# Optimization experiments

Hardware: AMD Instinct MI355X
Metric: run time of the kernel (lower is better)

Reference implementation:

```python
import jax, jax.numpy as jnp
import numpy as np

RADIUS = 0.1
NSAMPLE = 32


def ball_query_cnt(radius, nsample, xyz, new_xyz):
    """xyz: (B,N,3), new_xyz: (B,npoint,3) -> cnt (B,npoint) int32, idx (B,npoint,nsample) int32.
    Matches pointnet2 CUDA semantics: first `nsample` in-radius points in index order;
    unfilled slots replicate the first found index (0 if none found)."""
    N = xyz.shape[1]
    # (B, npoint, N) squared distances
    d2 = jnp.sum((new_xyz[:, :, None, :] - xyz[:, None, :, :]) ** 2, axis=-1)
    mask = d2 < radius * radius
    pos = jnp.arange(N, dtype=jnp.int32)
    # key encodes position so that top_k returns the LOWEST valid positions first
    key = jnp.where(mask, N - pos, -N)
    topk_vals, _ = jax.lax.top_k(key, nsample)          # (B, npoint, nsample)
    valid = topk_vals > 0
    idx = (N - topk_vals).astype(jnp.int32)
    first = jnp.where(valid[..., :1], idx[..., :1], 0)   # fill value per query
    idx = jnp.where(valid, idx, first)
    cnt = jnp.minimum(mask.sum(axis=-1), nsample).astype(jnp.int32)
    return cnt, idx


def group(features, idx):
    """features: (B,C,N), idx: (B,npoint,nsample) -> (B,C,npoint,nsample)."""
    return jax.vmap(lambda f, i: f[:, i])(features, idx)


def setup_inputs() -> dict:
    key = jax.random.key(0)
    k1, k2, k3 = jax.random.split(key, 3)
    B, N, npoint, C = 4, 16384, 2048, 64
    xyz = jax.random.uniform(k1, (B, N, 3), dtype=jnp.float32)
    new_xyz = jax.random.uniform(k2, (B, npoint, 3), dtype=jnp.float32)
    features = jax.random.normal(k3, (B, C, N), dtype=jnp.float32)
    return {"xyz": xyz, "new_xyz": new_xyz, "features": features}


def reference(xyz, new_xyz, features):
    idx_cnt, idx = ball_query_cnt(RADIUS, NSAMPLE, xyz, new_xyz)
    xyz_t = jnp.transpose(xyz, (0, 2, 1))                      # (B,3,N)
    grouped_xyz = group(xyz_t, idx)                            # (B,3,npoint,nsample)
    grouped_xyz = grouped_xyz - jnp.transpose(new_xyz, (0, 2, 1))[..., None]
    grouped_features = group(features, idx)                    # (B,C,npoint,nsample)
    new_features = jnp.concatenate([grouped_xyz, grouped_features], axis=1)
    return idx_cnt, new_features
```

## Files before the change

kernel.cpp:

```cpp
#include <hip/hip_runtime.h>

#define B        4
#define N        16384
#define NPOINT   2048
#define C        64
#define NSAMPLE  32
#define CH       (C + 3)
#define RADIUS2  0.01f
#define NCELL    1000
#define CSTRIDE  1032
#define CAP      256

#define WAVE_FENCE() asm volatile("s_waitcnt lgkmcnt(0)" ::: "memory")

__device__ __forceinline__ int clamp10(int v) {
    return v < 0 ? 0 : (v > 9 ? 9 : v);
}

__device__ __forceinline__ int cell_of(float x, float y, float z) {
    return (clamp10((int)(x * 10.f)) * 10 + clamp10((int)(y * 10.f))) * 10
         + clamp10((int)(z * 10.f));
}

__device__ __forceinline__ void transpose_body(const float* __restrict__ f,
                                               float* __restrict__ ft,
                                               int n0, int b, int t,
                                               float (*tile)[65]) {
    const int r16 = t >> 4;
    const int x4  = t & 15;
    #pragma unroll
    for (int it = 0; it < 4; ++it) {
        const int cc = it * 16 + r16;
        const float4 v = *(const float4*)(f + ((size_t)b * C + cc) * N + n0 + x4 * 4);
        tile[cc][x4 * 4 + 0] = v.x;
        tile[cc][x4 * 4 + 1] = v.y;
        tile[cc][x4 * 4 + 2] = v.z;
        tile[cc][x4 * 4 + 3] = v.w;
    }
    __syncthreads();
    #pragma unroll
    for (int it = 0; it < 4; ++it) {
        const int nn = it * 16 + r16;
        float4 v;
        v.x = tile[x4 * 4 + 0][nn];
        v.y = tile[x4 * 4 + 1][nn];
        v.z = tile[x4 * 4 + 2][nn];
        v.w = tile[x4 * 4 + 3][nn];
        *(float4*)(ft + ((size_t)b * N + n0 + nn) * C + x4 * 4) = v;
    }
}

__global__ __launch_bounds__(256) void prep2_kernel(
    const float*  __restrict__ xyz,
    const float*  __restrict__ f,
    float*        __restrict__ ft,
    int*          __restrict__ cs,
    float4*       __restrict__ sp)
{
    __shared__ int   cnts[1024];
    __shared__ int   wsum[4];
    __shared__ float tile[64][65];
    const int t = threadIdx.x;

    if (blockIdx.x < B) {
        const int b = blockIdx.x;
        const float* xb = xyz + (size_t)b * N * 3;

        for (int i = t; i < 1024; i += 256) cnts[i] = 0;
        __syncthreads();

        for (int i = t; i < N; i += 256) {
            const float x = xb[i * 3 + 0], y = xb[i * 3 + 1], z = xb[i * 3 + 2];
            atomicAdd(&cnts[cell_of(x, y, z)], 1);
        }
        __syncthreads();

        const int base4 = t * 4;
        const int a0 = cnts[base4 + 0], a1 = cnts[base4 + 1];
        const int a2 = cnts[base4 + 2], a3 = cnts[base4 + 3];
        const int s  = a0 + a1 + a2 + a3;
        const int w  = t >> 6, l = t & 63;
        int inc = s;
        #pragma unroll
        for (int off = 1; off < 64; off <<= 1) {
            const int u = __shfl_up(inc, off);
            if (l >= off) inc += u;
        }
        if (l == 63) wsum[w] = inc;
        __syncthreads();
        int wbase = 0;
        #pragma unroll
        for (int k = 0; k < 4; ++k) wbase += (k < w) ? wsum[k] : 0;
        const int e0 = wbase + inc - s;
        const int e1 = e0 + a0, e2 = e1 + a1, e3 = e2 + a2;
        cnts[base4 + 0] = e0;
        cnts[base4 + 1] = e1;
        cnts[base4 + 2] = e2;
        cnts[base4 + 3] = e3;
        int* csb = cs + b * CSTRIDE;
        csb[base4 + 0] = e0;
        csb[base4 + 1] = e1;
        csb[base4 + 2] = e2;
        csb[base4 + 3] = e3;
        __syncthreads();

        float4* spb = sp + ((size_t)b << 14);
        for (int i = t; i < N; i += 256) {
            const float x = xb[i * 3 + 0], y = xb[i * 3 + 1], z = xb[i * 3 + 2];
            const int pos = atomicAdd(&cnts[cell_of(x, y, z)], 1);
            spb[pos] = make_float4(x, y, z, __int_as_float(i));
        }
    } else {
        const int bi = blockIdx.x - B;
        transpose_body(f, ft, (bi & 255) * 64, bi >> 8, t, tile);
    }
}

__global__ __launch_bounds__(256) void feat_transpose_kernel(
    const float* __restrict__ f, float* __restrict__ ft) {
    __shared__ float tile[64][65];
    transpose_body(f, ft, blockIdx.x * 64, blockIdx.y, threadIdx.x, tile);
}

__global__ __launch_bounds__(256, 6) void qg_fused_kernel(
    const float*  __restrict__ xyz,
    const float*  __restrict__ new_xyz,
    const float*  __restrict__ ft,
    const int*    __restrict__ cs,
    const float4* __restrict__ sp,
    float* __restrict__ out_cnt,
    float* __restrict__ out_feat)
{
    const int w = threadIdx.x >> 6;
    const int l = threadIdx.x & 63;
    const int q = blockIdx.x * 4 + w;
    const int b = q >> 11;
    const int j = q & (NPOINT - 1);

    __shared__ int   cand_s[4][CAP];
    __shared__ int   si_s[4][NSAMPLE];
    __shared__ float tile_s[4][35 * 33];
    int*   cand = cand_s[w];
    int*   s_i  = si_s[w];
    float* tile = tile_s[w];

    const float qx = new_xyz[q * 3 + 0];
    const float qy = new_xyz[q * 3 + 1];
    const float qz = new_xyz[q * 3 + 2];

    const int cx = clamp10((int)(qx * 10.f));
    const int cy = clamp10((int)(qy * 10.f));
    const int cz = clamp10((int)(qz * 10.f));
    const int z0 = cz > 0 ? cz - 1 : 0;
    const int z1 = cz < 9 ? cz + 1 : 9;

    int sv = 0, ev = 0;
    if (l < 9) {
        const int xx = cx - 1 + l / 3;
        const int yy = cy - 1 + l % 3;
        if (xx >= 0 && xx <= 9 && yy >= 0 && yy <= 9) {
            const int cb = (xx * 10 + yy) * 10;
            sv = cs[b * CSTRIDE + cb + z0];
            ev = cs[b * CSTRIDE + cb + z1 + 1];
        }
    }

    const unsigned long long ltmask = (1ull << l) - 1ull;
    int total = 0, ncand = 0;
    for (int r = 0; r < 9; ++r) {
        const int rs = __shfl(sv, r);
        const int re = __shfl(ev, r);
        for (int p0 = rs; p0 < re; p0 += 64) {
            const int p = p0 + l;
            const bool act = p < re;
            float4 pt = make_float4(1e9f, 1e9f, 1e9f, 0.f);
            if (act) pt = sp[(b << 14) + p];
            const float dx = pt.x - qx, dy = pt.y - qy, dz = pt.z - qz;
            const float d2 = dx * dx + dy * dy + dz * dz;
            const bool in = act && (d2 < RADIUS2);
            const unsigned long long m = __ballot(in);
            if (in) {
                const int slot = ncand + __popcll(m & ltmask);
                if (slot < CAP) cand[slot] = __float_as_int(pt.w);
            }
            const int c = __popcll(m);
            total += c;
            ncand = ncand + c > CAP ? CAP : ncand + c;
        }
    }
    WAVE_FENCE();

    int cntv;
    if (total > CAP) {
        const float* xb = xyz + (size_t)b * N * 3;
        int cnt2 = 0;
        for (int base = 0; base < N; base += 64) {
            const int p = base + l;
            const float dx = xb[p * 3 + 0] - qx;
            const float dy = xb[p * 3 + 1] - qy;
            const float dz = xb[p * 3 + 2] - qz;
            const float d2 = dx * dx + dy * dy + dz * dz;
            const bool in = d2 < RADIUS2;
            const unsigned long long m = __ballot(in);
            if (in) {
                const int slot = cnt2 + __popcll(m & ltmask);
                if (slot < NSAMPLE) s_i[slot] = p;
            }
            cnt2 += __popcll(m);
            if (cnt2 >= NSAMPLE) break;
        }
        cntv = cnt2 < NSAMPLE ? cnt2 : NSAMPLE;
    } else {
        const int K = ncand;
        for (int c = l; c < K; c += 64) {
            const int v = cand[c];
            int rnk = 0;
            for (int i = 0; i < K; ++i) rnk += (cand[i] < v) ? 1 : 0;
            if (rnk < NSAMPLE) s_i[rnk] = v;
        }
        cntv = total < NSAMPLE ? total : NSAMPLE;
    }
    WAVE_FENCE();

    if (l == 0) out_cnt[q] = (float)cntv;
    if (l < NSAMPLE && l >= cntv) s_i[l] = (cntv > 0) ? s_i[0] : 0;
    WAVE_FENCE();

    if (l < NSAMPLE) {
        const int i = s_i[l];
        const float* xp = xyz + ((size_t)b * N + i) * 3;
        tile[0 * 33 + l] = xp[0] - qx;
        tile[1 * 33 + l] = xp[1] - qy;
        tile[2 * 33 + l] = xp[2] - qz;
    }
    const float4* ft4 = (const float4*)ft;
    #pragma unroll
    for (int t = 0; t < 4; ++t) {
        const int k  = t * 8 + (l >> 3);
        const int c4 = l & 7;
        const float4 v = ft4[((size_t)b * N + s_i[k]) * (C / 4) + c4];
        const int ch = 3 + c4 * 4;
        tile[(ch + 0) * 33 + k] = v.x;
        tile[(ch + 1) * 33 + k] = v.y;
        tile[(ch + 2) * 33 + k] = v.z;
        tile[(ch + 3) * 33 + k] = v.w;
    }
    WAVE_FENCE();

    float4* of4 = (float4*)out_feat;
    #pragma unroll
    for (int t = 0; t < 5; ++t) {
        const int e4 = t * 64 + l;
        if (e4 < 35 * 8) {
            const int ch = e4 >> 3;
            const int k4 = e4 & 7;
            float4 v;
            v.x = tile[ch * 33 + k4 * 4 + 0];
            v.y = tile[ch * 33 + k4 * 4 + 1];
            v.z = tile[ch * 33 + k4 * 4 + 2];
            v.w = tile[ch * 33 + k4 * 4 + 3];
            of4[((size_t)(b * CH + ch) * NPOINT + j) * 8 + k4] = v;
        }
    }
    WAVE_FENCE();

    #pragma unroll
    for (int t = 0; t < 4; ++t) {
        const int k  = t * 8 + (l >> 3);
        const int c4 = 8 + (l & 7);
        const float4 v = ft4[((size_t)b * N + s_i[k]) * (C / 4) + c4];
        const int r = (c4 - 8) * 4;
        tile[(r + 0) * 33 + k] = v.x;
        tile[(r + 1) * 33 + k] = v.y;
        tile[(r + 2) * 33 + k] = v.z;
        tile[(r + 3) * 33 + k] = v.w;
    }
    WAVE_FENCE();

    #pragma unroll
    for (int t = 0; t < 4; ++t) {
        const int e4  = t * 64 + l;
        const int chr = e4 >> 3;
        const int k4  = e4 & 7;
        float4 v;
        v.x = tile[chr * 33 + k4 * 4 + 0];
        v.y = tile[chr * 33 + k4 * 4 + 1];
        v.z = tile[chr * 33 + k4 * 4 + 2];
        v.w = tile[chr * 33 + k4 * 4 + 3];
        of4[((size_t)(b * CH + 35 + chr) * NPOINT + j) * 8 + k4] = v;
    }
}

template <bool TRANSPOSED>
__global__ __launch_bounds__(64) void qg_wave_kernel(
    const float* __restrict__ xyz,
    const float* __restrict__ new_xyz,
    const float* __restrict__ feat,
    float* __restrict__ out_cnt,
    float* __restrict__ out_feat)
{
    const int q = blockIdx.x;
    const int b = q >> 11;
    const int j = q & (NPOINT - 1);
    const int l = threadIdx.x;

    __shared__ int   s_idx[NSAMPLE];
    __shared__ float s_tile[CH * 33];

    const float qx = new_xyz[q * 3 + 0];
    const float qy = new_xyz[q * 3 + 1];
    const float qz = new_xyz[q * 3 + 2];
    const float* xb = xyz + (size_t)b * N * 3;

    int cnt = 0;
    for (int base = 0; base < N; base += 64) {
        const int p = base + l;
        const float dx = xb[p * 3 + 0] - qx;
        const float dy = xb[p * 3 + 1] - qy;
        const float dz = xb[p * 3 + 2] - qz;
        const float d2 = dx * dx + dy * dy + dz * dz;
        const bool in = d2 < RADIUS2;
        const unsigned long long m = __ballot(in);
        if (in) {
            const int slot = cnt + __popcll(m & ((1ull << l) - 1ull));
            if (slot < NSAMPLE) s_idx[slot] = p;
        }
        cnt += __popcll(m);
        if (cnt >= NSAMPLE) break;
    }
    if (cnt > NSAMPLE) cnt = NSAMPLE;

    if (l == 0) out_cnt[q] = (float)cnt;
    __syncthreads();
    if (l < NSAMPLE && l >= cnt) s_idx[l] = (cnt > 0) ? s_idx[0] : 0;
    __syncthreads();

    #pragma unroll
    for (int p = 0; p < 8; ++p) {
        const int k  = p * 4 + (l >> 4);
        const int c4 = l & 15;
        const int i  = s_idx[k];
        if (TRANSPOSED) {
            const float4 v = ((const float4*)(feat + ((size_t)b * N + i) * C))[c4];
            const int ch = 3 + c4 * 4;
            s_tile[(ch + 0) * 33 + k] = v.x;
            s_tile[(ch + 1) * 33 + k] = v.y;
            s_tile[(ch + 2) * 33 + k] = v.z;
            s_tile[(ch + 3) * 33 + k] = v.w;
        } else {
            #pragma unroll
            for (int cc = 0; cc < 4; ++cc) {
                const int c = c4 * 4 + cc;
                s_tile[(3 + c) * 33 + k] = feat[((size_t)b * C + c) * N + i];
            }
        }
    }
    if (l < NSAMPLE) {
        const int i = s_idx[l];
        const float* xp = xyz + ((size_t)b * N + i) * 3;
        s_tile[0 * 33 + l] = xp[0] - qx;
        s_tile[1 * 33 + l] = xp[1] - qy;
        s_tile[2 * 33 + l] = xp[2] - qz;
    }
    __syncthreads();

    float4* of4 = (float4*)out_feat;
    for (int e4 = l; e4 < CH * 8; e4 += 64) {
        const int ch = e4 >> 3;
        const int k4 = e4 & 7;
        float4 v;
        v.x = s_tile[ch * 33 + k4 * 4 + 0];
        v.y = s_tile[ch * 33 + k4 * 4 + 1];
        v.z = s_tile[ch * 33 + k4 * 4 + 2];
        v.w = s_tile[ch * 33 + k4 * 4 + 3];
        of4[((size_t)(b * CH + ch) * NPOINT + j) * 8 + k4] = v;
    }
}

extern "C" void kernel_launch(void* const* d_in, const int* in_sizes, int n_in,
                              void* d_out, int out_size, void* d_ws, size_t ws_size,
                              hipStream_t stream) {
    const float* xyz      = (const float*)d_in[0];
    const float* new_xyz  = (const float*)d_in[1];
    const float* features = (const float*)d_in[2];

    float* out_cnt  = (float*)d_out;
    float* out_feat = out_cnt + (size_t)B * NPOINT;

    char* ws = (char*)d_ws;
    const size_t ftB = (size_t)B * N * C * sizeof(float);
    const size_t spB = (size_t)B * N * sizeof(float4);
    const size_t csB = (size_t)B * CSTRIDE * sizeof(int);
    const size_t need = ftB + spB + csB;

    if (ws_size >= need) {
        float*  ft = (float*)ws;
        float4* sp = (float4*)(ws + ftB);
        int*    cs = (int*)(ws + ftB + spB);
        prep2_kernel<<<B + B * (N / 64), 256, 0, stream>>>(xyz, features, ft, cs, sp);
        qg_fused_kernel<<<B * NPOINT / 4, 256, 0, stream>>>(xyz, new_xyz, ft, cs, sp,
                                                            out_cnt, out_feat);
    } else if (ws_size >= ftB) {
        float* ft = (float*)ws;
        feat_transpose_kernel<<<dim3(N / 64, B), 256, 0, stream>>>(features, ft);
        qg_wave_kernel<true><<<B * NPOINT, 64, 0, stream>>>(xyz, new_xyz, ft,
                                                            out_cnt, out_feat);
    } else {
        qg_wave_kernel<false><<<B * NPOINT, 64, 0, stream>>>(xyz, new_xyz, features,
                                                             out_cnt, out_feat);
    }
}
```

Baseline: 153.8 us.

## Split grid build into parallel count/prefix/scatter kernels and prefetch first cell chunks

After: 136.1 us. 1.13x faster.

```diff
diff --git a/kernel.cpp b/kernel.cpp
--- a/kernel.cpp
+++ b/kernel.cpp
@@ -22,6 +22,11 @@
          + clamp10((int)(z * 10.f));
 }
 
+__global__ __launch_bounds__(256) void zero_kernel(int* __restrict__ p, int n) {
+    const int i = blockIdx.x * 256 + threadIdx.x;
+    if (i < n) p[i] = 0;
+}
+
 __device__ __forceinline__ void transpose_body(const float* __restrict__ f,
                                                float* __restrict__ ft,
                                                int n0, int b, int t,
@@ -50,69 +55,19 @@
     }
 }
 
-__global__ __launch_bounds__(256) void prep2_kernel(
-    const float*  __restrict__ xyz,
-    const float*  __restrict__ f,
-    float*        __restrict__ ft,
-    int*          __restrict__ cs,
-    float4*       __restrict__ sp)
-{
-    __shared__ int   cnts[1024];
-    __shared__ int   wsum[4];
+__global__ __launch_bounds__(256) void prep_kernel(const float* __restrict__ xyz,
+                                                   int* __restrict__ cnt,
+                                                   const float* __restrict__ f,
+                                                   float* __restrict__ ft) {
     __shared__ float tile[64][65];
-    const int t = threadIdx.x;
-
-    if (blockIdx.x < B) {
-        const int b = blockIdx.x;
-        const float* xb = xyz + (size_t)b * N * 3;
-
-        for (int i = t; i < 1024; i += 256) cnts[i] = 0;
-        __syncthreads();
-
-        for (int i = t; i < N; i += 256) {
-            const float x = xb[i * 3 + 0], y = xb[i * 3 + 1], z = xb[i * 3 + 2];
-            atomicAdd(&cnts[cell_of(x, y, z)], 1);
-        }
-        __syncthreads();
-
-        const int base4 = t * 4;
-        const int a0 = cnts[base4 + 0], a1 = cnts[base4 + 1];
-        const int a2 = cnts[base4 + 2], a3 = cnts[base4 + 3];
-        const int s  = a0 + a1 + a2 + a3;
-        const int w  = t >> 6, l = t & 63;
-        int inc = s;
-        #pragma unroll
-        for (int off = 1; off < 64; off <<= 1) {
-            const int u = __shfl_up(inc, off);
-            if (l >= off) inc += u;
-        }
-        if (l == 63) wsum[w] = inc;
-        __syncthreads();
-        int wbase = 0;
-        #pragma unroll
-        for (int k = 0; k < 4; ++k) wbase += (k < w) ? wsum[k] : 0;
-        const int e0 = wbase + inc - s;
-        const int e1 = e0 + a0, e2 = e1 + a1, e3 = e2 + a2;
-        cnts[base4 + 0] = e0;
-        cnts[base4 + 1] = e1;
-        cnts[base4 + 2] = e2;
-        cnts[base4 + 3] = e3;
-        int* csb = cs + b * CSTRIDE;
-        csb[base4 + 0] = e0;
-        csb[base4 + 1] = e1;
-        csb[base4 + 2] = e2;
-        csb[base4 + 3] = e3;
-        __syncthreads();
-
-        float4* spb = sp + ((size_t)b << 14);
-        for (int i = t; i < N; i += 256) {
-            const float x = xb[i * 3 + 0], y = xb[i * 3 + 1], z = xb[i * 3 + 2];
-            const int pos = atomicAdd(&cnts[cell_of(x, y, z)], 1);
-            spb[pos] = make_float4(x, y, z, __int_as_float(i));
-        }
+    if (blockIdx.x < (B * N / 256)) {
+        const int g = blockIdx.x * 256 + threadIdx.x;
+        const int b = g >> 14;
+        const float x = xyz[g * 3 + 0], y = xyz[g * 3 + 1], z = xyz[g * 3 + 2];
+        atomicAdd(&cnt[(b << 10) + cell_of(x, y, z)], 1);
     } else {
-        const int bi = blockIdx.x - B;
-        transpose_body(f, ft, (bi & 255) * 64, bi >> 8, t, tile);
+        const int bi = blockIdx.x - (B * N / 256);
+        transpose_body(f, ft, (bi & 255) * 64, bi >> 8, threadIdx.x, tile);
     }
 }
 
@@ -120,6 +75,47 @@
     const float* __restrict__ f, float* __restrict__ ft) {
     __shared__ float tile[64][65];
     transpose_body(f, ft, blockIdx.x * 64, blockIdx.y, threadIdx.x, tile);
+}
+
+__global__ __launch_bounds__(1024) void prefix_kernel(int* __restrict__ cnt,
+                                                      int* __restrict__ cs) {
+    __shared__ int wsum[16];
+    const int t = threadIdx.x, b = blockIdx.x;
+    const int w = t >> 6, l = t & 63;
+    const int v = (t < NCELL) ? cnt[(b << 10) + t] : 0;
+    int inc = v;
+    #pragma unroll
+    for (int off = 1; off < 64; off <<= 1) {
+        const int u = __shfl_up(inc, off);
+        if (l >= off) inc += u;
+    }
+    if (l == 63) wsum[w] = inc;
+    __syncthreads();
+    if (t < 16) {
+        int s = wsum[t];
+        #pragma unroll
+        for (int off = 1; off < 16; off <<= 1) {
+            const int u = __shfl_up(s, off, 16);
+            if (t >= off) s += u;
+        }
+        wsum[t] = s;
+    }
+    __syncthreads();
+    const int base = (w > 0) ? wsum[w - 1] : 0;
+    const int excl = base + inc - v;
+    if (t <= NCELL) cs[b * CSTRIDE + t] = excl;
+    if (t < NCELL)  cnt[(b << 10) + t] = excl;
+}
+
+__global__ __launch_bounds__(256) void scatter_kernel(const float* __restrict__ xyz,
+                                                      int* __restrict__ cursor,
+                                                      float4* __restrict__ sp) {
+    const int g = blockIdx.x * 256 + threadIdx.x;
+    const int b = g >> 14;
+    const int n = g & (N - 1);
+    const float x = xyz[g * 3 + 0], y = xyz[g * 3 + 1], z = xyz[g * 3 + 2];
+    const int pos = atomicAdd(&cursor[(b << 10) + cell_of(x, y, z)], 1);
+    sp[(b << 14) + pos] = make_float4(x, y, z, __int_as_float(n));
 }
 
 __global__ __launch_bounds__(256, 6) void qg_fused_kernel(
@@ -164,24 +160,54 @@
             ev = cs[b * CSTRIDE + cb + z1 + 1];
         }
     }
+    int rs[9], re[9];
+    #pragma unroll
+    for (int r = 0; r < 9; ++r) {
+        rs[r] = __shfl(sv, r);
+        re[r] = __shfl(ev, r);
+    }
 
     const unsigned long long ltmask = (1ull << l) - 1ull;
+    const float4* spb = sp + ((size_t)b << 14);
+
+    float4 pt[9];
+    bool   a[9];
+    #pragma unroll
+    for (int r = 0; r < 9; ++r) {
+        const int p = rs[r] + l;
+        a[r] = p < re[r];
+        pt[r] = a[r] ? spb[p] : make_float4(1e9f, 1e9f, 1e9f, 0.f);
+    }
     int total = 0, ncand = 0;
+    #pragma unroll
     for (int r = 0; r < 9; ++r) {
-        const int rs = __shfl(sv, r);
-        const int re = __shfl(ev, r);
-        for (int p0 = rs; p0 < re; p0 += 64) {
+        const float dx = pt[r].x - qx, dy = pt[r].y - qy, dz = pt[r].z - qz;
+        const float d2 = dx * dx + dy * dy + dz * dz;
+        const bool in = a[r] && (d2 < RADIUS2);
+        const unsigned long long m = __ballot(in);
+        if (in) {
+            const int slot = ncand + __popcll(m & ltmask);
+            if (slot < CAP) cand[slot] = __float_as_int(pt[r].w);
+        }
+        const int c = __popcll(m);
+        total += c;
+        ncand = ncand + c > CAP ? CAP : ncand + c;
+    }
+    #pragma unroll 1
+    for (int r = 0; r < 9; ++r) {
+        #pragma unroll 1
+        for (int p0 = rs[r] + 64; p0 < re[r]; p0 += 64) {
             const int p = p0 + l;
-            const bool act = p < re;
-            float4 pt = make_float4(1e9f, 1e9f, 1e9f, 0.f);
-            if (act) pt = sp[(b << 14) + p];
-            const float dx = pt.x - qx, dy = pt.y - qy, dz = pt.z - qz;
+            const bool act = p < re[r];
+            float4 pv = make_float4(1e9f, 1e9f, 1e9f, 0.f);
+            if (act) pv = spb[p];
+            const float dx = pv.x - qx, dy = pv.y - qy, dz = pv.z - qz;
             const float d2 = dx * dx + dy * dy + dz * dz;
             const bool in = act && (d2 < RADIUS2);
             const unsigned long long m = __ballot(in);
             if (in) {
                 const int slot = ncand + __popcll(m & ltmask);
-                if (slot < CAP) cand[slot] = __float_as_int(pt.w);
+                if (slot < CAP) cand[slot] = __float_as_int(pv.w);
             }
             const int c = __popcll(m);
             total += c;
@@ -349,8 +375,8 @@
             s_tile[(ch + 3) * 33 + k] = v.w;
         } else {
             #pragma unroll
-            for (int cc = 0; cc < 4; ++cc) {
-                const int c = c4 * 4 + cc;
+            for (int cc2 = 0; cc2 < 4; ++cc2) {
+                const int c = c4 * 4 + cc2;
                 s_tile[(3 + c) * 33 + k] = feat[((size_t)b * C + c) * N + i];
             }
         }
@@ -391,13 +417,19 @@
     const size_t ftB = (size_t)B * N * C * sizeof(float);
     const size_t spB = (size_t)B * N * sizeof(float4);
     const size_t csB = (size_t)B * CSTRIDE * sizeof(int);
-    const size_t need = ftB + spB + csB;
+    const size_t ccB = (size_t)B * 1024 * sizeof(int);
+    const size_t need = ftB + spB + csB + ccB;
 
     if (ws_size >= need) {
         float*  ft = (float*)ws;
         float4* sp = (float4*)(ws + ftB);
         int*    cs = (int*)(ws + ftB + spB);
-        prep2_kernel<<<B + B * (N / 64), 256, 0, stream>>>(xyz, features, ft, cs, sp);
+        int*    cc = (int*)(ws + ftB + spB + csB);
+        zero_kernel<<<(B * 1024 + 255) / 256, 256, 0, stream>>>(cc, B * 1024);
+        prep_kernel<<<(B * N / 256) + B * (N / 64), 256, 0, stream>>>(xyz, cc,
+                                                                      features, ft);
+        prefix_kernel<<<B, 1024, 0, stream>>>(cc, cs);
+        scatter_kernel<<<B * N / 256, 256, 0, stream>>>(xyz, cc, sp);
         qg_fused_kernel<<<B * NPOINT / 4, 256, 0, stream>>>(xyz, new_xyz, ft, cs, sp,
                                                             out_cnt, out_feat);
     } else if (ws_size >= ftB) {
```
